# Performance work log

Hardware: AMD Instinct MI355X
Metric: run time of the kernel (lower is better)

## Reference

```python
import jax, jax.numpy as jnp
import numpy as np

WIN = 4          # ka_win_num (2x2 grid of windows)
KS = 3           # kernel_size
HEADS = 8
PAD = 1


def setup_inputs() -> dict:
    key = jax.random.key(0)
    ks = jax.random.split(key, 11)
    B, res, C = 8, 256, 64
    c16 = C // 16  # SE bottleneck (dim >= 64 branch)
    inp = {
        "x": jax.random.normal(ks[0], (B, res * res, C), dtype=jnp.float32),
        # per-window grouped-conv weights (the "kernels" fed to attention)
        "conv_w": jax.random.normal(ks[1], (WIN, C, C, KS, KS), dtype=jnp.float32) * 0.05,
        "qkv_w": jax.random.normal(ks[2], (C, 3 * C), dtype=jnp.float32) * 0.05,
        "qkv_b": jax.random.normal(ks[3], (3 * C,), dtype=jnp.float32) * 0.01,
        "proj_w": jax.random.normal(ks[4], (C, C), dtype=jnp.float32) * 0.05,
        "proj_b": jax.random.normal(ks[5], (C,), dtype=jnp.float32) * 0.01,
        # per-window SE params (1x1 convs on pooled (k,k))
        "se_w1": jax.random.normal(ks[6], (WIN, c16, C), dtype=jnp.float32) * 0.1,
        "se_b1": jax.random.normal(ks[7], (WIN, c16), dtype=jnp.float32) * 0.01,
        "se_w2": jax.random.normal(ks[8], (WIN, C, c16), dtype=jnp.float32) * 0.1,
        "se_b2": jax.random.normal(ks[9], (WIN, C), dtype=jnp.float32) * 0.01,
    }
    return inp


def reference(x, conv_w, qkv_w, qkv_b, proj_w, proj_b, se_w1, se_b1, se_w2, se_b2):
    B, L, C = x.shape
    H = int(round(np.sqrt(L)))
    g = int(round(np.sqrt(WIN)))      # windows per side = 2
    ws = H // g                       # window_size
    hd = C // HEADS
    scale = hd ** (-0.5)
    S = WIN * KS * KS                 # attention sequence length

    xw = x.reshape(B, g, ws, g, ws, C).transpose(1, 3, 0, 5, 2, 4)
    xw = xw.reshape(WIN, B, C, ws, ws)

    # ---- gather conv kernels as tokens: weight.view(out,in,k2).permute(0,2,1), concat over windows
    kern_tok = conv_w.reshape(WIN, C, C, KS * KS).transpose(1, 0, 3, 2).reshape(C, S, C)

    # ---- self-attention over kernel tokens (batch = C_out = dim)
    qkv = kern_tok @ qkv_w + qkv_b                                    # (C, S, 3C)
    qkv = qkv.reshape(C, S, 3, HEADS, hd).transpose(2, 0, 3, 1, 4)     # (3, C, H, S, hd)
    q, kk, v = qkv[0] * scale, qkv[1], qkv[2]
    attn = jax.nn.softmax(jnp.einsum('chsd,chtd->chst', q, kk), axis=-1)
    out = jnp.einsum('chst,chtd->chsd', attn, v)                       # (C, H, S, hd)
    out = out.transpose(0, 2, 1, 3).reshape(C, S, C)
    out = out @ proj_w + proj_b

    kern = out.reshape(C, WIN, KS, KS, C).transpose(1, 0, 4, 2, 3)

    # ---- SE over each window's kernel, treating (C_out, C_in, k, k) as (N, Ch, H, W)
    pool = kern.mean(axis=(-2, -1))
    h = jax.nn.relu(jnp.einsum('wnc,wdc->wnd', pool, se_w1) + se_b1[:, None, :])
    s = jax.nn.sigmoid(jnp.einsum('wnd,wcd->wnc', h, se_w2) + se_b2[:, None, :])
    kern = kern * s[..., None, None]

    def conv(xi, wi):
        return jax.lax.conv_general_dilated(xi, wi, (1, 1), [(PAD, PAD), (PAD, PAD)])

    y = jax.vmap(conv)(xw, kern)

    y = y.reshape(g, g, B, C, ws, ws).transpose(2, 0, 4, 1, 5, 3).reshape(B, H * H, C)
    return y
```

## Files before the change

kernel.cpp:

```cpp
#include <hip/hip_runtime.h>
#include <hip/hip_bf16.h>

typedef __bf16 bf16x8 __attribute__((ext_vector_type(8)));
typedef float  f32x4  __attribute__((ext_vector_type(4)));

__global__ __launch_bounds__(192) void qkv_kernel(
    const float* __restrict__ conv_w, const float* __restrict__ qkv_w,
    const float* __restrict__ qkv_b,
    float* __restrict__ qv, float* __restrict__ kvv, float* __restrict__ vv)
{
    __shared__ float tok[64];
    const int bid = blockIdx.x;
    const int co = bid / 36, s = bid - co * 36;
    const int w = s / 9, p = s - w * 9;
    const int t = threadIdx.x;
    if (t < 64) tok[t] = conv_w[(((w * 64 + co) * 64 + t) * 9) + p];
    __syncthreads();
    float acc = qkv_b[t];
#pragma unroll 8
    for (int ci = 0; ci < 64; ++ci) acc += tok[ci] * qkv_w[ci * 192 + t];
    const int trip = t >> 6, rem = t & 63, h = rem >> 3, d = rem & 7;
    if (trip == 0) acc *= 0.35355339059327373f;
    float* dst = (trip == 0) ? qv : ((trip == 1) ? kvv : vv);
    dst[((co * 8 + h) * 36 + s) * 8 + d] = acc;
}

__global__ __launch_bounds__(64) void attn_kernel(
    const float* __restrict__ qv, const float* __restrict__ kvv,
    const float* __restrict__ vv, float* __restrict__ ao)
{
    __shared__ float kl[288], vl[288];
    const int bid = blockIdx.x;
    const int t = threadIdx.x;
    const float* kb = kvv + bid * 288;
    const float* vb = vv + bid * 288;
    for (int i = t; i < 288; i += 64) { kl[i] = kb[i]; vl[i] = vb[i]; }
    __syncthreads();
    if (t < 36) {
        float q[8];
        const float* qb = qv + bid * 288 + t * 8;
#pragma unroll
        for (int d = 0; d < 8; ++d) q[d] = qb[d];
        float sc[36];
        float mx = -1e30f;
#pragma unroll
        for (int u = 0; u < 36; ++u) {
            float a = 0.f;
#pragma unroll
            for (int d = 0; d < 8; ++d) a += q[d] * kl[u * 8 + d];
            sc[u] = a;
            mx = fmaxf(mx, a);
        }
        float sum = 0.f;
        float o[8] = {0.f,0.f,0.f,0.f,0.f,0.f,0.f,0.f};
#pragma unroll
        for (int u = 0; u < 36; ++u) {
            float e = expf(sc[u] - mx);
            sum += e;
#pragma unroll
            for (int d = 0; d < 8; ++d) o[d] += e * vl[u * 8 + d];
        }
        const float inv = 1.0f / sum;
        const int co = bid >> 3, h = bid & 7;
        float* dst = ao + (co * 36 + t) * 64 + h * 8;
#pragma unroll
        for (int d = 0; d < 8; ++d) dst[d] = o[d] * inv;
    }
}

__global__ __launch_bounds__(64) void proj_se_kernel(
    const float* __restrict__ ao, const float* __restrict__ proj_w,
    const float* __restrict__ proj_b,
    const float* __restrict__ se_w1, const float* __restrict__ se_b1,
    const float* __restrict__ se_w2, const float* __restrict__ se_b2,
    ushort* __restrict__ kout)
{
    __shared__ float al[9][64];
    __shared__ float pool[64];
    __shared__ float hb[4];
    const int bid = blockIdx.x;
    const int w = bid >> 6, co = bid & 63;
    const int t = threadIdx.x;
    for (int i = t; i < 576; i += 64) {
        int p = i >> 6, j = i & 63;
        al[p][j] = ao[(co * 36 + w * 9 + p) * 64 + j];
    }
    __syncthreads();
    float kv[9];
#pragma unroll
    for (int p = 0; p < 9; ++p) {
        float a = proj_b[t];
#pragma unroll 8
        for (int j = 0; j < 64; ++j) a += al[p][j] * proj_w[j * 64 + t];
        kv[p] = a;
    }
    float pl = 0.f;
#pragma unroll
    for (int p = 0; p < 9; ++p) pl += kv[p];
    pool[t] = pl * (1.0f / 9.0f);
    __syncthreads();
    if (t < 4) {
        float hh = se_b1[w * 4 + t];
#pragma unroll 8
        for (int c = 0; c < 64; ++c) hh += pool[c] * se_w1[(w * 4 + t) * 64 + c];
        hb[t] = fmaxf(hh, 0.0f);
    }
    __syncthreads();
    float z = se_b2[w * 64 + t];
#pragma unroll
    for (int d = 0; d < 4; ++d) z += hb[d] * se_w2[(w * 64 + t) * 4 + d];
    const float sg = 1.0f / (1.0f + expf(-z));
    const int hhalf = t >> 5, ci32 = t & 31;
#pragma unroll
    for (int p = 0; p < 9; ++p) {
        __hip_bfloat16 hv = __float2bfloat16(kv[p] * sg);
        kout[(((hhalf * 4 + w) * 9) + p) * 2048 + co * 32 + ci32] = *(const ushort*)&hv;
    }
}

__global__ __launch_bounds__(256, 3) void conv_kernel(
    const float* __restrict__ x, const ushort* __restrict__ kern,
    float* __restrict__ out)
{
    __shared__ alignas(16) ushort in_lds[18 * 18 * 64];
    __shared__ alignas(16) ushort kn_lds[3 * 2048];

    const int tid = threadIdx.x;

    const int bid = blockIdx.x;
    const int nb  = ((bid & 7) << 8) + (bid >> 3);
    const int bz  = nb >> 6;
    const int rem = nb & 63;
    const int i0  = (rem >> 3) << 4;
    const int j0  = (rem & 7) << 4;
    const int w = bz >> 3, b = bz & 7;
    const int gi = w >> 1, gj = w & 1;

    const int wv   = tid >> 6;
    const int lane = tid & 63;
    const int l15  = lane & 15;
    const int hi4  = lane >> 4;

    const char* kern_b = (const char*)kern;
    const int ksrc = (lane << 4) ^ (((lane >> 3) & 3) << 4);
    auto stage_kern = [&](int s, int buf) {
        const int p = s >> 1, hh = s & 1;
        const char* gs = kern_b + ((size_t)((((hh * 4 + w) * 9)) + p) << 12);
        __builtin_amdgcn_global_load_lds(
            (const __attribute__((address_space(1))) unsigned int*)(gs + (wv << 10) + ksrc),
            (__attribute__((address_space(3))) unsigned int*)
                ((char*)kn_lds + (buf << 12) + (wv << 10)),
            16, 0, 0);
    };

    stage_kern(0, 0);
    stage_kern(1, 1);

    {
        const int cc = (tid & 15) << 2;
        const int p0 = tid >> 4;
        float4 v[21];
        unsigned okm = 0;
#pragma unroll
        for (int k = 0; k < 21; ++k) {
            const int pp = p0 + (k << 4);
            const int ppc = pp < 323 ? pp : 323;
            const int r = ppc / 18, q = ppc - r * 18;
            const int iy = i0 - 1 + r, jx = j0 - 1 + q;
            const bool ok = (pp < 324) & (iy >= 0) & (iy < 128) & (jx >= 0) & (jx < 128);
            const int iyc = iy < 0 ? 0 : (iy > 127 ? 127 : iy);
            const int jxc = jx < 0 ? 0 : (jx > 127 ? 127 : jx);
            const size_t xi = (((size_t)b << 16) +
                               (size_t)(gi * 128 + iyc) * 256 + (size_t)(gj * 128 + jxc)) * 64 + cc;
            v[k] = *(const float4*)(x + xi);
            okm |= (unsigned)ok << k;
        }
#pragma unroll
        for (int k = 0; k < 21; ++k) {
            const int pp = p0 + (k << 4);
            if (pp < 324) {
                const int r = pp / 18, q = pp - r * 18;
                float4 z = (okm >> k) & 1 ? v[k] : make_float4(0.f, 0.f, 0.f, 0.f);
                union { ushort4 u; ushort h4[4]; } tmp;
                __hip_bfloat16 b0 = __float2bfloat16(z.x); tmp.h4[0] = *(const ushort*)&b0;
                __hip_bfloat16 b1 = __float2bfloat16(z.y); tmp.h4[1] = *(const ushort*)&b1;
                __hip_bfloat16 b2 = __float2bfloat16(z.z); tmp.h4[2] = *(const ushort*)&b2;
                __hip_bfloat16 b3 = __float2bfloat16(z.w); tmp.h4[3] = *(const ushort*)&b3;
                *(ushort4*)((char*)in_lds +
                    ((pp << 7) + ((cc << 1) ^ ((q & 7) << 4)))) = tmp.u;
            }
        }
    }

    f32x4 acc[4][4];
#pragma unroll
    for (int mf = 0; mf < 4; ++mf)
#pragma unroll
        for (int nf = 0; nf < 4; ++nf)
            acc[mf][nf] = (f32x4){0.f, 0.f, 0.f, 0.f};

    __syncthreads();

#pragma unroll
    for (int s = 0; s < 18; ++s) {
        asm volatile("s_waitcnt vmcnt(1)" ::: "memory");
        __builtin_amdgcn_sched_barrier(0);
        __builtin_amdgcn_s_barrier();
        __builtin_amdgcn_sched_barrier(0);

        const int buf = s % 3;
        const int p = s >> 1, hh = s & 1;
        const int kh = p / 3, kw = p - kh * 3;

        bf16x8 Kf[4];
#pragma unroll
        for (int nf = 0; nf < 4; ++nf) {
            const int co = nf * 16 + l15;
            Kf[nf] = *(const bf16x8*)((const char*)kn_lds +
                      ((buf << 12) + (co << 6) +
                       ((hi4 << 4) ^ (((co >> 1) & 3) << 4))));
        }

        const int q = l15 + kw;
        const int swz = (q & 7) << 4;
        const int c2 = (hh << 6) | (hi4 << 4);
#pragma unroll
        for (int mf = 0; mf < 4; ++mf) {
            const int r = wv * 4 + mf + kh;
            bf16x8 Af = *(const bf16x8*)((const char*)in_lds +
                          (((r * 18 + q) << 7) + (c2 ^ swz)));
#pragma unroll
            for (int nf = 0; nf < 4; ++nf)
                acc[mf][nf] = __builtin_amdgcn_mfma_f32_16x16x32_bf16(
                    Kf[nf], Af, acc[mf][nf], 0, 0, 0);
        }

        if (s < 16) stage_kern(s + 2, (s + 2) % 3);
    }

    asm volatile("s_waitcnt lgkmcnt(0)" ::: "memory");
    __builtin_amdgcn_sched_barrier(0);
    __builtin_amdgcn_s_barrier();
    __builtin_amdgcn_sched_barrier(0);

    char* ep = (char*)in_lds + (wv << 12);
#pragma unroll
    for (int mf = 0; mf < 4; ++mf) {
        const int iloc = wv * 4 + mf;
        const size_t rowoff = ((size_t)b << 16) +
                              (size_t)(gi * 128 + i0 + iloc) * 256 + (size_t)(gj * 128 + j0);
#pragma unroll
        for (int nf = 0; nf < 4; ++nf) {
            const int off = (nf * 64 + hi4 * 16) ^ ((l15 & 7) << 4);
            *(f32x4*)(ep + l15 * 256 + off) = acc[mf][nf];
        }
#pragma unroll
        for (int t = 0; t < 4; ++t) {
            const int px = t * 4 + hi4;
            f32x4 vv4 = *(const f32x4*)(ep + px * 256 + ((l15 << 4) ^ ((px & 7) << 4)));
            *(f32x4*)(out + (rowoff + px) * 64 + l15 * 4) = vv4;
        }
    }
}

extern "C" void kernel_launch(void* const* d_in, const int* in_sizes, int n_in,
                              void* d_out, int out_size, void* d_ws, size_t ws_size,
                              hipStream_t stream)
{
    const float* x      = (const float*)d_in[0];
    const float* conv_w = (const float*)d_in[1];
    const float* qkv_w  = (const float*)d_in[2];
    const float* qkv_b  = (const float*)d_in[3];
    const float* proj_w = (const float*)d_in[4];
    const float* proj_b = (const float*)d_in[5];
    const float* se_w1  = (const float*)d_in[6];
    const float* se_b1  = (const float*)d_in[7];
    const float* se_w2  = (const float*)d_in[8];
    const float* se_b2  = (const float*)d_in[9];
    float* out = (float*)d_out;

    float* qv = (float*)d_ws;
    float* kv = qv + 147456;
    float* vv = kv + 147456;
    float* ao = vv + 147456;
    ushort* kb = (ushort*)(ao + 147456);

    hipLaunchKernelGGL(qkv_kernel, dim3(2304), dim3(192), 0, stream,
                       conv_w, qkv_w, qkv_b, qv, kv, vv);
    hipLaunchKernelGGL(attn_kernel, dim3(512), dim3(64), 0, stream, qv, kv, vv, ao);
    hipLaunchKernelGGL(proj_se_kernel, dim3(256), dim3(64), 0, stream,
                       ao, proj_w, proj_b, se_w1, se_b1, se_w2, se_b2, kb);
    hipLaunchKernelGGL(conv_kernel, dim3(2048), dim3(256), 0, stream, x, kb, out);
}
```

Baseline: 84.23 us.

## Load conv kernel fragments directly into registers instead of staging through LDS

```diff
diff --git a/kernel.cpp b/kernel.cpp
--- a/kernel.cpp
+++ b/kernel.cpp
@@ -123,7 +123,6 @@
     float* __restrict__ out)
 {
     __shared__ alignas(16) ushort in_lds[18 * 18 * 64];
-    __shared__ alignas(16) ushort kn_lds[3 * 2048];
 
     const int tid = threadIdx.x;
 
@@ -141,20 +140,22 @@
     const int l15  = lane & 15;
     const int hi4  = lane >> 4;
 
-    const char* kern_b = (const char*)kern;
-    const int ksrc = (lane << 4) ^ (((lane >> 3) & 3) << 4);
-    auto stage_kern = [&](int s, int buf) {
+    const ushort* kwl = kern + l15 * 32 + hi4 * 8;
+    auto kchunk = [&](int s) -> const ushort* {
         const int p = s >> 1, hh = s & 1;
-        const char* gs = kern_b + ((size_t)((((hh * 4 + w) * 9)) + p) << 12);
-        __builtin_amdgcn_global_load_lds(
-            (const __attribute__((address_space(1))) unsigned int*)(gs + (wv << 10) + ksrc),
-            (__attribute__((address_space(3))) unsigned int*)
-                ((char*)kn_lds + (buf << 12) + (wv << 10)),
-            16, 0, 0);
+        return kwl + ((((hh * 4 + w) * 9) + p) << 11);
     };
 
-    stage_kern(0, 0);
-    stage_kern(1, 1);
+    bf16x8 K[3][4];
+
+    {
+        const ushort* g0 = kchunk(0);
+        const ushort* g1 = kchunk(1);
+#pragma unroll
+        for (int nf = 0; nf < 4; ++nf) K[0][nf] = *(const bf16x8*)(g0 + nf * 512);
+#pragma unroll
+        for (int nf = 0; nf < 4; ++nf) K[1][nf] = *(const bf16x8*)(g1 + nf * 512);
+    }
 
     {
         const int cc = (tid & 15) << 2;
@@ -203,24 +204,15 @@
 
 #pragma unroll
     for (int s = 0; s < 18; ++s) {
-        asm volatile("s_waitcnt vmcnt(1)" ::: "memory");
-        __builtin_amdgcn_sched_barrier(0);
-        __builtin_amdgcn_s_barrier();
-        __builtin_amdgcn_sched_barrier(0);
-
-        const int buf = s % 3;
+        if (s < 16) {
+            const ushort* gs = kchunk(s + 2);
+#pragma unroll
+            for (int nf = 0; nf < 4; ++nf)
+                K[(s + 2) % 3][nf] = *(const bf16x8*)(gs + nf * 512);
+        }
+
         const int p = s >> 1, hh = s & 1;
         const int kh = p / 3, kw = p - kh * 3;
-
-        bf16x8 Kf[4];
-#pragma unroll
-        for (int nf = 0; nf < 4; ++nf) {
-            const int co = nf * 16 + l15;
-            Kf[nf] = *(const bf16x8*)((const char*)kn_lds +
-                      ((buf << 12) + (co << 6) +
-                       ((hi4 << 4) ^ (((co >> 1) & 3) << 4))));
-        }
-
         const int q = l15 + kw;
         const int swz = (q & 7) << 4;
         const int c2 = (hh << 6) | (hi4 << 4);
@@ -232,16 +224,11 @@
 #pragma unroll
             for (int nf = 0; nf < 4; ++nf)
                 acc[mf][nf] = __builtin_amdgcn_mfma_f32_16x16x32_bf16(
-                    Kf[nf], Af, acc[mf][nf], 0, 0, 0);
-        }
-
-        if (s < 16) stage_kern(s + 2, (s + 2) % 3);
-    }
-
-    asm volatile("s_waitcnt lgkmcnt(0)" ::: "memory");
-    __builtin_amdgcn_sched_barrier(0);
-    __builtin_amdgcn_s_barrier();
-    __builtin_amdgcn_sched_barrier(0);
+                    K[s % 3][nf], Af, acc[mf][nf], 0, 0, 0);
+        }
+    }
+
+    __syncthreads();
 
     char* ep = (char*)in_lds + (wv << 12);
 #pragma unroll
```

After: 140.2 us. 1.66x slower.

## Split input-tile load by channel half and overlap second half with MFMA loop

Applied to the files above, without the earlier changes.

```diff
diff --git a/kernel.cpp b/kernel.cpp
--- a/kernel.cpp
+++ b/kernel.cpp
@@ -144,7 +144,8 @@
     const char* kern_b = (const char*)kern;
     const int ksrc = (lane << 4) ^ (((lane >> 3) & 3) << 4);
     auto stage_kern = [&](int s, int buf) {
-        const int p = s >> 1, hh = s & 1;
+        const int hh = (s < 9) ? 0 : 1;
+        const int p  = (s < 9) ? s : s - 9;
         const char* gs = kern_b + ((size_t)((((hh * 4 + w) * 9)) + p) << 12);
         __builtin_amdgcn_global_load_lds(
             (const __attribute__((address_space(1))) unsigned int*)(gs + (wv << 10) + ksrc),
@@ -153,17 +154,64 @@
             16, 0, 0);
     };
 
+    const int cc = (tid & 7) << 2;
+    const int p0 = tid >> 3;
+
+    float4 hold[3];
+    unsigned okm = 0;
+
+    auto issue_inp1 = [&](int kbeg, int kend) {
+        okm = 0;
+#pragma unroll
+        for (int k = kbeg; k < kend; ++k) {
+            const int pp = p0 + (k << 5);
+            const int ppc = pp < 323 ? pp : 323;
+            const int r = ppc / 18, q = ppc - r * 18;
+            const int iy = i0 - 1 + r, jx = j0 - 1 + q;
+            const bool ok = (pp < 324) & (iy >= 0) & (iy < 128) & (jx >= 0) & (jx < 128);
+            const int iyc = iy < 0 ? 0 : (iy > 127 ? 127 : iy);
+            const int jxc = jx < 0 ? 0 : (jx > 127 ? 127 : jx);
+            const size_t xi = (((size_t)b << 16) +
+                               (size_t)(gi * 128 + iyc) * 256 + (size_t)(gj * 128 + jxc)) * 64 +
+                              32 + cc;
+            hold[k - kbeg] = *(const float4*)(x + xi);
+            okm |= (unsigned)ok << (k - kbeg);
+        }
+    };
+    auto write_inp1 = [&](int kbeg, int kend) {
+#pragma unroll
+        for (int k = kbeg; k < kend; ++k) {
+            const int pp = p0 + (k << 5);
+            if (pp < 324) {
+                const int r = pp / 18, q = pp - r * 18;
+                float4 z = (okm >> (k - kbeg)) & 1 ? hold[k - kbeg]
+                                                   : make_float4(0.f, 0.f, 0.f, 0.f);
+                union { ushort4 u; ushort h4[4]; } tmp;
+                __hip_bfloat16 b0 = __float2bfloat16(z.x); tmp.h4[0] = *(const ushort*)&b0;
+                __hip_bfloat16 b1 = __float2bfloat16(z.y); tmp.h4[1] = *(const ushort*)&b1;
+                __hip_bfloat16 b2 = __float2bfloat16(z.z); tmp.h4[2] = *(const ushort*)&b2;
+                __hip_bfloat16 b3 = __float2bfloat16(z.w); tmp.h4[3] = *(const ushort*)&b3;
+                *(ushort4*)((char*)in_lds +
+                    ((pp << 7) + (((1 << 6) + (cc << 1)) ^ ((q & 7) << 4)))) = tmp.u;
+            }
+        }
+    };
+
+    f32x4 acc[4][4];
+#pragma unroll
+    for (int mf = 0; mf < 4; ++mf)
+#pragma unroll
+        for (int nf = 0; nf < 4; ++nf)
+            acc[mf][nf] = (f32x4){0.f, 0.f, 0.f, 0.f};
+
     stage_kern(0, 0);
     stage_kern(1, 1);
-
     {
-        const int cc = (tid & 15) << 2;
-        const int p0 = tid >> 4;
-        float4 v[21];
-        unsigned okm = 0;
-#pragma unroll
-        for (int k = 0; k < 21; ++k) {
-            const int pp = p0 + (k << 4);
+        float4 v[11];
+        unsigned ok0 = 0;
+#pragma unroll
+        for (int k = 0; k < 11; ++k) {
+            const int pp = p0 + (k << 5);
             const int ppc = pp < 323 ? pp : 323;
             const int r = ppc / 18, q = ppc - r * 18;
             const int iy = i0 - 1 + r, jx = j0 - 1 + q;
@@ -173,14 +221,14 @@
             const size_t xi = (((size_t)b << 16) +
                                (size_t)(gi * 128 + iyc) * 256 + (size_t)(gj * 128 + jxc)) * 64 + cc;
             v[k] = *(const float4*)(x + xi);
-            okm |= (unsigned)ok << k;
-        }
-#pragma unroll
-        for (int k = 0; k < 21; ++k) {
-            const int pp = p0 + (k << 4);
+            ok0 |= (unsigned)ok << k;
+        }
+#pragma unroll
+        for (int k = 0; k < 11; ++k) {
+            const int pp = p0 + (k << 5);
             if (pp < 324) {
                 const int r = pp / 18, q = pp - r * 18;
-                float4 z = (okm >> k) & 1 ? v[k] : make_float4(0.f, 0.f, 0.f, 0.f);
+                float4 z = (ok0 >> k) & 1 ? v[k] : make_float4(0.f, 0.f, 0.f, 0.f);
                 union { ushort4 u; ushort h4[4]; } tmp;
                 __hip_bfloat16 b0 = __float2bfloat16(z.x); tmp.h4[0] = *(const ushort*)&b0;
                 __hip_bfloat16 b1 = __float2bfloat16(z.y); tmp.h4[1] = *(const ushort*)&b1;
@@ -191,25 +239,48 @@
             }
         }
     }
-
-    f32x4 acc[4][4];
-#pragma unroll
-    for (int mf = 0; mf < 4; ++mf)
-#pragma unroll
-        for (int nf = 0; nf < 4; ++nf)
-            acc[mf][nf] = (f32x4){0.f, 0.f, 0.f, 0.f};
-
     __syncthreads();
 
 #pragma unroll
     for (int s = 0; s < 18; ++s) {
-        asm volatile("s_waitcnt vmcnt(1)" ::: "memory");
+        if (s >= 1 && s <= 6)      asm volatile("s_waitcnt vmcnt(4)" ::: "memory");
+        else if (s == 7 || s == 8) asm volatile("s_waitcnt vmcnt(3)" ::: "memory");
+        else if (s >= 9)           asm volatile("s_waitcnt vmcnt(1)" ::: "memory");
         __builtin_amdgcn_sched_barrier(0);
+        if (s == 9) {
+            asm volatile("s_waitcnt lgkmcnt(0)" ::: "memory");
+            __builtin_amdgcn_sched_barrier(0);
+        }
         __builtin_amdgcn_s_barrier();
         __builtin_amdgcn_sched_barrier(0);
 
+        if (s < 16) stage_kern(s + 2, (s + 2) % 3);
+
+        if (s == 0) { issue_inp1(0, 3); }
+        else if (s == 2) {
+            asm volatile("s_waitcnt vmcnt(2)" ::: "memory");
+            __builtin_amdgcn_sched_barrier(0);
+            write_inp1(0, 3); issue_inp1(3, 6);
+        }
+        else if (s == 4) {
+            asm volatile("s_waitcnt vmcnt(2)" ::: "memory");
+            __builtin_amdgcn_sched_barrier(0);
+            write_inp1(3, 6); issue_inp1(6, 9);
+        }
+        else if (s == 6) {
+            asm volatile("s_waitcnt vmcnt(2)" ::: "memory");
+            __builtin_amdgcn_sched_barrier(0);
+            write_inp1(6, 9); issue_inp1(9, 11);
+        }
+        else if (s == 8) {
+            asm volatile("s_waitcnt vmcnt(2)" ::: "memory");
+            __builtin_amdgcn_sched_barrier(0);
+            write_inp1(9, 11);
+        }
+
         const int buf = s % 3;
-        const int p = s >> 1, hh = s & 1;
+        const int hh = (s < 9) ? 0 : 1;
+        const int p  = (s < 9) ? s : s - 9;
         const int kh = p / 3, kw = p - kh * 3;
 
         bf16x8 Kf[4];
@@ -234,14 +305,9 @@
                 acc[mf][nf] = __builtin_amdgcn_mfma_f32_16x16x32_bf16(
                     Kf[nf], Af, acc[mf][nf], 0, 0, 0);
         }
-
-        if (s < 16) stage_kern(s + 2, (s + 2) % 3);
-    }
-
-    asm volatile("s_waitcnt lgkmcnt(0)" ::: "memory");
-    __builtin_amdgcn_sched_barrier(0);
-    __builtin_amdgcn_s_barrier();
-    __builtin_amdgcn_sched_barrier(0);
+    }
+
+    __syncthreads();
 
     char* ep = (char*)in_lds + (wv << 12);
 #pragma unroll
```

After: 113.9 us. 1.35x slower.

## Stage full 64-channel kernel taps per pipeline step, halving barrier count

Applied to the files above, without the earlier changes.

```diff
diff --git a/kernel.cpp b/kernel.cpp
--- a/kernel.cpp
+++ b/kernel.cpp
@@ -110,20 +110,19 @@
 #pragma unroll
     for (int d = 0; d < 4; ++d) z += hb[d] * se_w2[(w * 64 + t) * 4 + d];
     const float sg = 1.0f / (1.0f + expf(-z));
-    const int hhalf = t >> 5, ci32 = t & 31;
 #pragma unroll
     for (int p = 0; p < 9; ++p) {
         __hip_bfloat16 hv = __float2bfloat16(kv[p] * sg);
-        kout[(((hhalf * 4 + w) * 9) + p) * 2048 + co * 32 + ci32] = *(const ushort*)&hv;
-    }
-}
-
-__global__ __launch_bounds__(256, 3) void conv_kernel(
+        kout[((w * 9 + p) * 64 + co) * 64 + t] = *(const ushort*)&hv;
+    }
+}
+
+__global__ __launch_bounds__(256, 2) void conv_kernel(
     const float* __restrict__ x, const ushort* __restrict__ kern,
     float* __restrict__ out)
 {
     __shared__ alignas(16) ushort in_lds[18 * 18 * 64];
-    __shared__ alignas(16) ushort kn_lds[3 * 2048];
+    __shared__ alignas(16) ushort kn_lds[3 * 4096];
 
     const int tid = threadIdx.x;
 
@@ -142,14 +141,20 @@
     const int hi4  = lane >> 4;
 
     const char* kern_b = (const char*)kern;
-    const int ksrc = (lane << 4) ^ (((lane >> 3) & 3) << 4);
-    auto stage_kern = [&](int s, int buf) {
-        const int p = s >> 1, hh = s & 1;
-        const char* gs = kern_b + ((size_t)((((hh * 4 + w) * 9)) + p) << 12);
+    const int ksrc8 = ((lane >> 3) & 7) << 4;
+    auto stage_kern = [&](int p, int buf) {
+        const char* gs = kern_b + ((size_t)(w * 9 + p) << 13);
+        const int woA = (wv << 11) + (lane << 4);
+        const int woB = woA + 1024;
         __builtin_amdgcn_global_load_lds(
-            (const __attribute__((address_space(1))) unsigned int*)(gs + (wv << 10) + ksrc),
+            (const __attribute__((address_space(1))) unsigned int*)(gs + (woA ^ ksrc8)),
             (__attribute__((address_space(3))) unsigned int*)
-                ((char*)kn_lds + (buf << 12) + (wv << 10)),
+                ((char*)kn_lds + (buf << 13) + woA),
+            16, 0, 0);
+        __builtin_amdgcn_global_load_lds(
+            (const __attribute__((address_space(1))) unsigned int*)(gs + (woB ^ ksrc8)),
+            (__attribute__((address_space(3))) unsigned int*)
+                ((char*)kn_lds + (buf << 13) + woB),
             16, 0, 0);
     };
 
@@ -202,40 +207,46 @@
     __syncthreads();
 
 #pragma unroll
-    for (int s = 0; s < 18; ++s) {
-        asm volatile("s_waitcnt vmcnt(1)" ::: "memory");
+    for (int s = 0; s < 9; ++s) {
+        if (s < 8) asm volatile("s_waitcnt vmcnt(2)" ::: "memory");
+        else       asm volatile("s_waitcnt vmcnt(0)" ::: "memory");
         __builtin_amdgcn_sched_barrier(0);
         __builtin_amdgcn_s_barrier();
         __builtin_amdgcn_sched_barrier(0);
 
+        if (s < 7) stage_kern(s + 2, (s + 2) % 3);
+
         const int buf = s % 3;
-        const int p = s >> 1, hh = s & 1;
-        const int kh = p / 3, kw = p - kh * 3;
-
-        bf16x8 Kf[4];
+        const int kh = s / 3, kw = s - kh * 3;
+
+        bf16x8 Kf[4][2];
 #pragma unroll
         for (int nf = 0; nf < 4; ++nf) {
             const int co = nf * 16 + l15;
-            Kf[nf] = *(const bf16x8*)((const char*)kn_lds +
-                      ((buf << 12) + (co << 6) +
-                       ((hi4 << 4) ^ (((co >> 1) & 3) << 4))));
+#pragma unroll
+            for (int ks = 0; ks < 2; ++ks)
+                Kf[nf][ks] = *(const bf16x8*)((const char*)kn_lds +
+                              ((buf << 13) + (co << 7) +
+                               (((ks << 6) | (hi4 << 4)) ^ ((co & 7) << 4))));
         }
 
         const int q = l15 + kw;
         const int swz = (q & 7) << 4;
-        const int c2 = (hh << 6) | (hi4 << 4);
 #pragma unroll
         for (int mf = 0; mf < 4; ++mf) {
             const int r = wv * 4 + mf + kh;
-            bf16x8 Af = *(const bf16x8*)((const char*)in_lds +
-                          (((r * 18 + q) << 7) + (c2 ^ swz)));
-#pragma unroll
-            for (int nf = 0; nf < 4; ++nf)
-                acc[mf][nf] = __builtin_amdgcn_mfma_f32_16x16x32_bf16(
-                    Kf[nf], Af, acc[mf][nf], 0, 0, 0);
-        }
-
-        if (s < 16) stage_kern(s + 2, (s + 2) % 3);
+            const int rowbase = (r * 18 + q) << 7;
+#pragma unroll
+            for (int ks = 0; ks < 2; ++ks) {
+                const int c2 = (ks << 6) | (hi4 << 4);
+                bf16x8 Af = *(const bf16x8*)((const char*)in_lds +
+                              (rowbase + (c2 ^ swz)));
+#pragma unroll
+                for (int nf = 0; nf < 4; ++nf)
+                    acc[mf][nf] = __builtin_amdgcn_mfma_f32_16x16x32_bf16(
+                        Kf[nf][ks], Af, acc[mf][nf], 0, 0, 0);
+            }
+        }
     }
 
     asm volatile("s_waitcnt lgkmcnt(0)" ::: "memory");
```

Result: slower. 87.26 us (+3.6%).
